# Kernel optimization log

Hardware: AMD Instinct MI355X
Metric: run time of the kernel (lower is better)

The kernel has to match this reference:

```python
import jax, jax.numpy as jnp
import numpy as np

MAX_VAL = 1000000000000.0


def setup_inputs() -> dict:
    key = jax.random.key(0)
    k1, k2, k3, k4 = jax.random.split(key, 4)
    B, H, N, D = 2, 16, 2048, 64
    query = jax.random.normal(k1, (B, H, N, D), dtype=jnp.float32)
    key_t = jax.random.normal(k2, (B, H, N, D), dtype=jnp.float32)
    value = jax.random.normal(k3, (B, H, N, D), dtype=jnp.float32)
    mask = jax.random.randint(k4, (B, 1, 1, N), 0, 2).astype(bool)
    return {"query": query, "key": key_t, "value": value, "mask": mask,
            "global_num": 8, "window_size": 64}


def reference(query, key, value, mask, global_num, window_size):
    # query/key/value: [B, H, N, D]; mask: [B, 1, 1, N] bool (True = keep)
    B, H, N, D = query.shape
    scale = 1.0 / jnp.sqrt(jnp.asarray(D, dtype=query.dtype))

    # split heads: first global_num are global, rest are local (windowed)
    q_g, k_g, v_g = query[:, :global_num], key[:, :global_num], value[:, :global_num]
    q_l, k_l, v_l = query[:, global_num:], key[:, global_num:], value[:, global_num:]

    # ---- global heads: dense masked attention ----
    scores_g = jnp.einsum('bhqd,bhkd->bhqk', q_g, k_g) * scale
    scores_g = jnp.where(mask, scores_g, -MAX_VAL)
    p_g = jax.nn.softmax(scores_g, axis=-1)
    out_g = jnp.einsum('bhqk,bhkd->bhqd', p_g, v_l[:, :0]) if False else jnp.einsum('bhqk,bhkd->bhqd', p_g, v_g)

    # ---- local heads: window-banded mask on top of padding mask ----
    pos = jnp.arange(N)
    distance = jnp.abs(pos[None, :] - pos[:, None])  # [N, N]
    band = (distance <= window_size)                 # [N, N] bool
    mask_l = mask & band                             # [B, 1, N, N]
    scores_l = jnp.einsum('bhqd,bhkd->bhqk', q_l, k_l) * scale
    scores_l = jnp.where(mask_l, scores_l, -MAX_VAL)
    p_l = jax.nn.softmax(scores_l, axis=-1)
    out_l = jnp.einsum('bhqk,bhkd->bhqd', p_l, v_l)

    out = jnp.concatenate([out_g, out_l], axis=1)  # [B, H, N, D]
    return (out, p_g, p_l)
```

## Files before the change

kernel.cpp:

```cpp
#include <hip/hip_runtime.h>
#include <stdint.h>

typedef __attribute__((ext_vector_type(8))) __bf16 bf16x8;
typedef __attribute__((ext_vector_type(4))) float f32x4;
typedef __attribute__((ext_vector_type(4))) int i32x4;

#define DEVI static __device__ __forceinline__

constexpr int NN = 2048;
constexpr int DD = 64;
constexpr int NH = 16;
constexpr int NG = 8;
constexpr float SCALE = 0.125f;
constexpr float NEGBIG = -1.0e12f;
constexpr size_t OUT_ELEMS = (size_t)2 * NH * NN * DD;
constexpr size_t PG_ELEMS  = (size_t)2 * NG * NN * NN;
constexpr size_t T_ELEMS   = (size_t)2 * NH * NN * DD;
constexpr size_t WS_NEED   = 5 * T_ELEMS * sizeof(__bf16);

struct Frag { bf16x8 hi, lo; };

DEVI Frag make_frag(const float* p) {
  f32x4 a = *(const f32x4*)p;
  f32x4 b = *(const f32x4*)(p + 4);
  Frag f;
#pragma unroll
  for (int j = 0; j < 8; j++) {
    float x = (j < 4) ? a[j] : b[j - 4];
    __bf16 h = (__bf16)x;
    f.hi[j] = h;
    f.lo[j] = (__bf16)(x - (float)h);
  }
  return f;
}

DEVI f32x4 mfma(bf16x8 a, bf16x8 b, f32x4 c) {
  return __builtin_amdgcn_mfma_f32_16x16x32_bf16(a, b, c, 0, 0, 0);
}

DEVI void compute_st(const Frag kf[2][2], const Frag* qf_rs, f32x4 acc[2]) {
#pragma unroll
  for (int Mt = 0; Mt < 2; Mt++) {
    f32x4 c = {0.f, 0.f, 0.f, 0.f};
#pragma unroll
    for (int ks = 0; ks < 2; ks++) {
      c = mfma(kf[Mt][ks].hi, qf_rs[ks].hi, c);
      c = mfma(kf[Mt][ks].hi, qf_rs[ks].lo, c);
      c = mfma(kf[Mt][ks].lo, qf_rs[ks].hi, c);
    }
    acc[Mt] = c;
  }
}

__global__ __launch_bounds__(256)
void prep(const float* __restrict__ Q, const float* __restrict__ K,
          const float* __restrict__ V, __bf16* __restrict__ W) {
  const int bid = blockIdx.x;
  if (bid < 4096) {
    const float* src = (bid < 2048) ? Q : K;
    __bf16* hi = W + ((bid < 2048) ? (size_t)0 : 2 * T_ELEMS);
    __bf16* lo = hi + T_ELEMS;
    const size_t base = ((size_t)(bid & 2047) * 256 + threadIdx.x) * 8;
    f32x4 a = *(const f32x4*)(src + base);
    f32x4 b = *(const f32x4*)(src + base + 4);
    bf16x8 h, l;
#pragma unroll
    for (int j = 0; j < 8; j++) {
      float x = (j < 4) ? a[j] : b[j - 4];
      __bf16 hh = (__bf16)x;
      h[j] = hh;
      l[j] = (__bf16)(x - (float)hh);
    }
    *(bf16x8*)(hi + base) = h;
    *(bf16x8*)(lo + base) = l;
  } else {
    __bf16* vt = W + 4 * T_ELEMS;
    const int t  = (bid - 4096) * 256 + (int)threadIdx.x;
    const int ng = t & 63;
    const int dh = t >> 6;
    const int d  = dh & 63;
    const int bh = dh >> 6;
    const float* vp = V + (size_t)bh * NN * DD;
    __bf16* dst = vt + ((size_t)bh * DD + d) * NN + ng * 32;
    bf16x8 o[4];
#pragma unroll
    for (int j = 0; j < 32; j++)
      o[j >> 3][j & 7] = (__bf16)vp[(size_t)(ng * 32 + j) * DD + d];
#pragma unroll
    for (int k = 0; k < 4; k++) *(bf16x8*)(dst + k * 8) = o[k];
  }
}

template <bool PRE>
__global__ __launch_bounds__(256, 2)
void wattn(const float* __restrict__ Q, const float* __restrict__ K,
           const float* __restrict__ V, const int* __restrict__ MSK,
           float* __restrict__ OUT, const __bf16* __restrict__ W) {
  const int bid = blockIdx.x;
  const bool loc = bid >= 256;
  const int lb = loc ? bid - 256 : bid;
  const int bh = lb >> 4;
  const int b  = bh >> 3;
  const int hh = bh & 7;
  const int h  = loc ? (hh + 8) : hh;
  const int wave = (int)(threadIdx.x >> 6);
  const int lane = (int)(threadIdx.x & 63);
  const int qi = lane >> 4;
  const int li = lane & 15;
  const int rb = (lb & 15) * 128 + wave * 32;

  const size_t tbase = ((size_t)(b * NH + h) * NN) * DD;
  const float* qp = Q + tbase;
  const float* kp = K + tbase;
  const float* vp = V + tbase;
  const __bf16* qhi = W + tbase;
  const __bf16* qlo = W + T_ELEMS + tbase;
  const __bf16* khi = W + 2 * T_ELEMS + tbase;
  const __bf16* klo = W + 3 * T_ELEMS + tbase;
  const __bf16* vt  = W + 4 * T_ELEMS + (size_t)(b * NH + h) * DD * NN;
  const int*   mp = MSK + (size_t)b * NN;
  float* op = OUT + tbase;
  float* pp = OUT + OUT_ELEMS + (loc ? PG_ELEMS : (size_t)0)
                  + ((size_t)(b * NG + hh) * NN) * NN;

  Frag qf[2][2];
#pragma unroll
  for (int rs = 0; rs < 2; rs++)
#pragma unroll
    for (int ks = 0; ks < 2; ks++) {
      const size_t off = (size_t)(rb + rs * 16 + li) * DD + ks * 32 + qi * 8;
      if constexpr (PRE) {
        qf[rs][ks].hi = *(const bf16x8*)(qhi + off);
        qf[rs][ks].lo = *(const bf16x8*)(qlo + off);
      } else {
        qf[rs][ks] = make_frag(qp + off);
      }
    }

  int wlo = 0, whi = 0;
  if (loc) {
    wlo = rb - 64; if (wlo < 0) wlo = 0;
    whi = rb + 96; if (whi > NN) whi = NN;
    const f32x4 z = {0.f, 0.f, 0.f, 0.f};
#pragma unroll 1
    for (int rr = 0; rr < 32; rr++) {
      float* dst = pp + (size_t)(rb + rr) * NN;
#pragma unroll 1
      for (int c = lane * 4; c < NN; c += 256) {
        if (c >= wlo && c < whi) continue;
        *(f32x4*)(dst + c) = z;
      }
    }
  }

  const int ntiles = loc ? 5 : 64;

  float m[2] = {NEGBIG, NEGBIG};
  float l[2] = {0.f, 0.f};

#pragma unroll 1
  for (int t = 0; t < ntiles; t++) {
    const int wc = loc ? (rb - 64 + 32 * t) : (32 * t);
    if (wc < 0 || wc >= NN) continue;

    Frag kf[2][2];
#pragma unroll
    for (int Mt = 0; Mt < 2; Mt++)
#pragma unroll
      for (int ks = 0; ks < 2; ks++) {
        const size_t off = (size_t)(wc + Mt * 16 + li) * DD + ks * 32 + qi * 8;
        if constexpr (PRE) {
          kf[Mt][ks].hi = *(const bf16x8*)(khi + off);
          kf[Mt][ks].lo = *(const bf16x8*)(klo + off);
        } else {
          kf[Mt][ks] = make_frag(kp + off);
        }
      }

    i32x4 mv[2];
    mv[0] = *(const i32x4*)(mp + wc + qi * 4);
    mv[1] = *(const i32x4*)(mp + wc + 16 + qi * 4);

#pragma unroll
    for (int rs = 0; rs < 2; rs++) {
      f32x4 acc[2];
      compute_st(kf, qf[rs], acc);
      const int row = rb + rs * 16 + li;
      float vals[8];
#pragma unroll
      for (int Mt = 0; Mt < 2; Mt++)
#pragma unroll
        for (int r = 0; r < 4; r++) {
          const int col = wc + Mt * 16 + qi * 4 + r;
          bool ok = (mv[Mt][r] != 0);
          if (loc) { int d = row - col; if (d < 0) d = -d; ok = ok && (d <= 64); }
          vals[Mt * 4 + r] = ok ? acc[Mt][r] * SCALE : NEGBIG;
        }
      float mx = vals[0];
#pragma unroll
      for (int j = 1; j < 8; j++) mx = fmaxf(mx, vals[j]);
      const float mn = fmaxf(m[rs], mx);
      float s = 0.f;
#pragma unroll
      for (int j = 0; j < 8; j++) s += __expf(vals[j] - mn);
      l[rs] = l[rs] * __expf(m[rs] - mn) + s;
      m[rs] = mn;
    }
  }

  float rl[2];
#pragma unroll
  for (int rs = 0; rs < 2; rs++) {
#pragma unroll
    for (int off = 16; off <= 32; off <<= 1) {
      const float mo = __shfl_xor(m[rs], off);
      const float lo2 = __shfl_xor(l[rs], off);
      const float mn = fmaxf(m[rs], mo);
      l[rs] = l[rs] * __expf(m[rs] - mn) + lo2 * __expf(mo - mn);
      m[rs] = mn;
    }
    rl[rs] = 1.0f / l[rs];
  }

  f32x4 o[2][4];
#pragma unroll
  for (int rs = 0; rs < 2; rs++)
#pragma unroll
    for (int dt = 0; dt < 4; dt++) o[rs][dt] = (f32x4){0.f, 0.f, 0.f, 0.f};

  const int srcA = (((qi * 2) + 0) & 3) * 16 + li;
  const int srcB = (((qi * 2) + 1) & 3) * 16 + li;
  const bool selB = (qi >> 1) != 0;

#pragma unroll 1
  for (int t = 0; t < ntiles; t++) {
    const int wc = loc ? (rb - 64 + 32 * t) : (32 * t);
    if (wc < 0 || wc >= NN) continue;

    Frag kf[2][2];
#pragma unroll
    for (int Mt = 0; Mt < 2; Mt++)
#pragma unroll
      for (int ks = 0; ks < 2; ks++) {
        const size_t off = (size_t)(wc + Mt * 16 + li) * DD + ks * 32 + qi * 8;
        if constexpr (PRE) {
          kf[Mt][ks].hi = *(const bf16x8*)(khi + off);
          kf[Mt][ks].lo = *(const bf16x8*)(klo + off);
        } else {
          kf[Mt][ks] = make_frag(kp + off);
        }
      }

    i32x4 mv[2];
    mv[0] = *(const i32x4*)(mp + wc + qi * 4);
    mv[1] = *(const i32x4*)(mp + wc + 16 + qi * 4);

    bf16x8 vf[4];
    if constexpr (PRE) {
#pragma unroll
      for (int dt = 0; dt < 4; dt++)
        vf[dt] = *(const bf16x8*)(vt + (size_t)(dt * 16 + li) * NN + wc + qi * 8);
    } else {
#pragma unroll
      for (int dt = 0; dt < 4; dt++)
#pragma unroll
        for (int j = 0; j < 8; j++)
          vf[dt][j] = (__bf16)vp[(size_t)(wc + qi * 8 + j) * DD + dt * 16 + li];
    }

#pragma unroll
    for (int rs = 0; rs < 2; rs++) {
      f32x4 acc[2];
      compute_st(kf, qf[rs], acc);
      const int row = rb + rs * 16 + li;
      float pf[8];
#pragma unroll
      for (int Mt = 0; Mt < 2; Mt++)
#pragma unroll
        for (int r = 0; r < 4; r++) {
          const int col = wc + Mt * 16 + qi * 4 + r;
          bool ok = (mv[Mt][r] != 0);
          if (loc) { int d = row - col; if (d < 0) d = -d; ok = ok && (d <= 64); }
          const float vv = ok ? acc[Mt][r] * SCALE : NEGBIG;
          pf[Mt * 4 + r] = __expf(vv - m[rs]) * rl[rs];
        }
      float pa[8];
#pragma unroll
      for (int j = 0; j < 8; j++) {
        const int src = (j < 4) ? srcA : srcB;
        const float v0 = __shfl(pf[0 + (j & 3)], src);
        const float v1 = __shfl(pf[4 + (j & 3)], src);
        pa[j] = selB ? v1 : v0;
      }
      float* prow = pp + (size_t)(rb + rs * 16 + li) * NN + wc + qi * 8;
      *(f32x4*)prow       = (f32x4){pa[0], pa[1], pa[2], pa[3]};
      *(f32x4*)(prow + 4) = (f32x4){pa[4], pa[5], pa[6], pa[7]};
      bf16x8 pb;
#pragma unroll
      for (int j = 0; j < 8; j++) pb[j] = (__bf16)pa[j];
#pragma unroll
      for (int dt = 0; dt < 4; dt++)
        o[rs][dt] = mfma(pb, vf[dt], o[rs][dt]);
    }
  }

#pragma unroll
  for (int rs = 0; rs < 2; rs++) {
#pragma unroll
    for (int dt = 0; dt < 4; dt++)
#pragma unroll
      for (int r = 0; r < 4; r++) {
        const int row = rb + rs * 16 + qi * 4 + r;
        op[(size_t)row * DD + dt * 16 + li] = o[rs][dt][r];
      }
  }
}

extern "C" void kernel_launch(void* const* d_in, const int* in_sizes, int n_in,
                              void* d_out, int out_size, void* d_ws, size_t ws_size,
                              hipStream_t stream) {
  (void)in_sizes; (void)n_in; (void)out_size;
  const float* Q = (const float*)d_in[0];
  const float* K = (const float*)d_in[1];
  const float* V = (const float*)d_in[2];
  const int*   M = (const int*)d_in[3];
  float* O = (float*)d_out;
  if (ws_size >= WS_NEED && d_ws != nullptr) {
    __bf16* W = (__bf16*)d_ws;
    prep<<<dim3(4608), dim3(256), 0, stream>>>(Q, K, V, W);
    wattn<true><<<dim3(512), dim3(256), 0, stream>>>(Q, K, V, M, O, W);
  } else {
    wattn<false><<<dim3(512), dim3(256), 0, stream>>>(Q, K, V, M, O, nullptr);
  }
}
```

Baseline: 784.0 us.

## Double-buffer K/V register tiles and specialize global vs local loops

Splits the attention loops into separate global and local paths, with the local band check made a compile-time template parameter. In the global path, K (and V) tiles plus the mask for the next step are loaded into a second register buffer while the current tile is computed, so global-memory latency overlaps with MFMA and softmax work. This raises register pressure, which could lower occupancy under the two-blocks-per-SM launch bound, and the last iteration issues a redundant reload.

```diff
diff --git a/kernel.cpp b/kernel.cpp
--- a/kernel.cpp
+++ b/kernel.cpp
@@ -38,17 +38,132 @@
   return __builtin_amdgcn_mfma_f32_16x16x32_bf16(a, b, c, 0, 0, 0);
 }
 
-DEVI void compute_st(const Frag kf[2][2], const Frag* qf_rs, f32x4 acc[2]) {
-#pragma unroll
-  for (int Mt = 0; Mt < 2; Mt++) {
-    f32x4 c = {0.f, 0.f, 0.f, 0.f};
+struct KT { bf16x8 hi[2][2]; bf16x8 lo[2][2]; i32x4 mv[2]; };
+struct VT { bf16x8 v[4]; };
+
+template <bool PRE>
+DEVI void load_kt(KT& kt, const __bf16* khi, const __bf16* klo,
+                  const float* kp, const int* mp, int wc, int li, int qi) {
+#pragma unroll
+  for (int Mt = 0; Mt < 2; Mt++)
 #pragma unroll
     for (int ks = 0; ks < 2; ks++) {
-      c = mfma(kf[Mt][ks].hi, qf_rs[ks].hi, c);
-      c = mfma(kf[Mt][ks].hi, qf_rs[ks].lo, c);
-      c = mfma(kf[Mt][ks].lo, qf_rs[ks].hi, c);
-    }
-    acc[Mt] = c;
+      const size_t off = (size_t)(wc + Mt * 16 + li) * DD + ks * 32 + qi * 8;
+      if constexpr (PRE) {
+        kt.hi[Mt][ks] = *(const bf16x8*)(khi + off);
+        kt.lo[Mt][ks] = *(const bf16x8*)(klo + off);
+      } else {
+        Frag f = make_frag(kp + off);
+        kt.hi[Mt][ks] = f.hi;
+        kt.lo[Mt][ks] = f.lo;
+      }
+    }
+  kt.mv[0] = *(const i32x4*)(mp + wc + qi * 4);
+  kt.mv[1] = *(const i32x4*)(mp + wc + 16 + qi * 4);
+}
+
+template <bool PRE>
+DEVI void load_vt(VT& vt, const __bf16* vtp, const float* vp, int wc, int li, int qi) {
+  if constexpr (PRE) {
+#pragma unroll
+    for (int dt = 0; dt < 4; dt++)
+      vt.v[dt] = *(const bf16x8*)(vtp + (size_t)(dt * 16 + li) * NN + wc + qi * 8);
+  } else {
+#pragma unroll
+    for (int dt = 0; dt < 4; dt++)
+#pragma unroll
+      for (int j = 0; j < 8; j++)
+        vt.v[dt][j] = (__bf16)vp[(size_t)(wc + qi * 8 + j) * DD + dt * 16 + li];
+  }
+}
+
+template <bool LOC>
+DEVI void tileA(const KT& kt, const Frag qf[2][2], int wc, int rb, int li, int qi,
+                float* m, float* l) {
+#pragma unroll
+  for (int rs = 0; rs < 2; rs++) {
+    f32x4 acc[2];
+#pragma unroll
+    for (int Mt = 0; Mt < 2; Mt++) {
+      f32x4 c = {0.f, 0.f, 0.f, 0.f};
+#pragma unroll
+      for (int ks = 0; ks < 2; ks++) {
+        c = mfma(kt.hi[Mt][ks], qf[rs][ks].hi, c);
+        c = mfma(kt.hi[Mt][ks], qf[rs][ks].lo, c);
+        c = mfma(kt.lo[Mt][ks], qf[rs][ks].hi, c);
+      }
+      acc[Mt] = c;
+    }
+    const int row = rb + rs * 16 + li;
+    float vals[8];
+#pragma unroll
+    for (int Mt = 0; Mt < 2; Mt++)
+#pragma unroll
+      for (int r = 0; r < 4; r++) {
+        const int col = wc + Mt * 16 + qi * 4 + r;
+        bool ok = (kt.mv[Mt][r] != 0);
+        if constexpr (LOC) { int d = row - col; if (d < 0) d = -d; ok = ok && (d <= 64); }
+        vals[Mt * 4 + r] = ok ? acc[Mt][r] * SCALE : NEGBIG;
+      }
+    float mx = vals[0];
+#pragma unroll
+    for (int j = 1; j < 8; j++) mx = fmaxf(mx, vals[j]);
+    const float mn = fmaxf(m[rs], mx);
+    float s = 0.f;
+#pragma unroll
+    for (int j = 0; j < 8; j++) s += __expf(vals[j] - mn);
+    l[rs] = l[rs] * __expf(m[rs] - mn) + s;
+    m[rs] = mn;
+  }
+}
+
+template <bool LOC>
+DEVI void tileB(const KT& kt, const VT& vt, const Frag qf[2][2], int wc, int rb,
+                int li, int qi, const float* m, const float* rl,
+                f32x4 (&o)[2][4], float* pp, int srcA, int srcB, bool selB) {
+#pragma unroll
+  for (int rs = 0; rs < 2; rs++) {
+    f32x4 acc[2];
+#pragma unroll
+    for (int Mt = 0; Mt < 2; Mt++) {
+      f32x4 c = {0.f, 0.f, 0.f, 0.f};
+#pragma unroll
+      for (int ks = 0; ks < 2; ks++) {
+        c = mfma(kt.hi[Mt][ks], qf[rs][ks].hi, c);
+        c = mfma(kt.hi[Mt][ks], qf[rs][ks].lo, c);
+        c = mfma(kt.lo[Mt][ks], qf[rs][ks].hi, c);
+      }
+      acc[Mt] = c;
+    }
+    const int row = rb + rs * 16 + li;
+    float pf[8];
+#pragma unroll
+    for (int Mt = 0; Mt < 2; Mt++)
+#pragma unroll
+      for (int r = 0; r < 4; r++) {
+        const int col = wc + Mt * 16 + qi * 4 + r;
+        bool ok = (kt.mv[Mt][r] != 0);
+        if constexpr (LOC) { int d = row - col; if (d < 0) d = -d; ok = ok && (d <= 64); }
+        const float vv = ok ? acc[Mt][r] * SCALE : NEGBIG;
+        pf[Mt * 4 + r] = __expf(vv - m[rs]) * rl[rs];
+      }
+    float pa[8];
+#pragma unroll
+    for (int j = 0; j < 8; j++) {
+      const int src = (j < 4) ? srcA : srcB;
+      const float v0 = __shfl(pf[0 + (j & 3)], src);
+      const float v1 = __shfl(pf[4 + (j & 3)], src);
+      pa[j] = selB ? v1 : v0;
+    }
+    float* prow = pp + (size_t)(rb + rs * 16 + li) * NN + wc + qi * 8;
+    *(f32x4*)prow       = (f32x4){pa[0], pa[1], pa[2], pa[3]};
+    *(f32x4*)(prow + 4) = (f32x4){pa[4], pa[5], pa[6], pa[7]};
+    bf16x8 pb;
+#pragma unroll
+    for (int j = 0; j < 8; j++) pb[j] = (__bf16)pa[j];
+#pragma unroll
+    for (int dt = 0; dt < 4; dt++)
+      o[rs][dt] = mfma(pb, vt.v[dt], o[rs][dt]);
   }
 }
 
@@ -109,17 +224,17 @@
   const int li = lane & 15;
   const int rb = (lb & 15) * 128 + wave * 32;
 
-  const size_t tbase = ((size_t)(b * NH + h) * NN) * DD;
-  const float* qp = Q + tbase;
-  const float* kp = K + tbase;
-  const float* vp = V + tbase;
-  const __bf16* qhi = W + tbase;
-  const __bf16* qlo = W + T_ELEMS + tbase;
-  const __bf16* khi = W + 2 * T_ELEMS + tbase;
-  const __bf16* klo = W + 3 * T_ELEMS + tbase;
-  const __bf16* vt  = W + 4 * T_ELEMS + (size_t)(b * NH + h) * DD * NN;
+  const size_t tb = ((size_t)(b * NH + h) * NN) * DD;
+  const float* qp = Q + tb;
+  const float* kp = K + tb;
+  const float* vp = V + tb;
+  const __bf16* qhi = W + tb;
+  const __bf16* qlo = W + T_ELEMS + tb;
+  const __bf16* khi = W + 2 * T_ELEMS + tb;
+  const __bf16* klo = W + 3 * T_ELEMS + tb;
+  const __bf16* vtp = W + 4 * T_ELEMS + (size_t)(b * NH + h) * DD * NN;
   const int*   mp = MSK + (size_t)b * NN;
-  float* op = OUT + tbase;
+  float* op = OUT + tb;
   float* pp = OUT + OUT_ELEMS + (loc ? PG_ELEMS : (size_t)0)
                   + ((size_t)(b * NG + hh) * NN) * NN;
 
@@ -137,10 +252,23 @@
       }
     }
 
-  int wlo = 0, whi = 0;
-  if (loc) {
-    wlo = rb - 64; if (wlo < 0) wlo = 0;
-    whi = rb + 96; if (whi > NN) whi = NN;
+  float m[2] = {NEGBIG, NEGBIG};
+  float l[2] = {0.f, 0.f};
+
+  if (!loc) {
+    KT ka, kb;
+    load_kt<PRE>(ka, khi, klo, kp, mp, 0, li, qi);
+#pragma unroll 1
+    for (int t = 0; t < 64; t += 2) {
+      load_kt<PRE>(kb, khi, klo, kp, mp, (t + 1) * 32, li, qi);
+      tileA<false>(ka, qf, t * 32, rb, li, qi, m, l);
+      const int wn = (t + 2 < 64) ? (t + 2) * 32 : 63 * 32;
+      load_kt<PRE>(ka, khi, klo, kp, mp, wn, li, qi);
+      tileA<false>(kb, qf, (t + 1) * 32, rb, li, qi, m, l);
+    }
+  } else {
+    int wlo = rb - 64; if (wlo < 0) wlo = 0;
+    int whi = rb + 96; if (whi > NN) whi = NN;
     const f32x4 z = {0.f, 0.f, 0.f, 0.f};
 #pragma unroll 1
     for (int rr = 0; rr < 32; rr++) {
@@ -151,60 +279,13 @@
         *(f32x4*)(dst + c) = z;
       }
     }
-  }
-
-  const int ntiles = loc ? 5 : 64;
-
-  float m[2] = {NEGBIG, NEGBIG};
-  float l[2] = {0.f, 0.f};
-
-#pragma unroll 1
-  for (int t = 0; t < ntiles; t++) {
-    const int wc = loc ? (rb - 64 + 32 * t) : (32 * t);
-    if (wc < 0 || wc >= NN) continue;
-
-    Frag kf[2][2];
-#pragma unroll
-    for (int Mt = 0; Mt < 2; Mt++)
-#pragma unroll
-      for (int ks = 0; ks < 2; ks++) {
-        const size_t off = (size_t)(wc + Mt * 16 + li) * DD + ks * 32 + qi * 8;
-        if constexpr (PRE) {
-          kf[Mt][ks].hi = *(const bf16x8*)(khi + off);
-          kf[Mt][ks].lo = *(const bf16x8*)(klo + off);
-        } else {
-          kf[Mt][ks] = make_frag(kp + off);
-        }
-      }
-
-    i32x4 mv[2];
-    mv[0] = *(const i32x4*)(mp + wc + qi * 4);
-    mv[1] = *(const i32x4*)(mp + wc + 16 + qi * 4);
-
-#pragma unroll
-    for (int rs = 0; rs < 2; rs++) {
-      f32x4 acc[2];
-      compute_st(kf, qf[rs], acc);
-      const int row = rb + rs * 16 + li;
-      float vals[8];
-#pragma unroll
-      for (int Mt = 0; Mt < 2; Mt++)
-#pragma unroll
-        for (int r = 0; r < 4; r++) {
-          const int col = wc + Mt * 16 + qi * 4 + r;
-          bool ok = (mv[Mt][r] != 0);
-          if (loc) { int d = row - col; if (d < 0) d = -d; ok = ok && (d <= 64); }
-          vals[Mt * 4 + r] = ok ? acc[Mt][r] * SCALE : NEGBIG;
-        }
-      float mx = vals[0];
-#pragma unroll
-      for (int j = 1; j < 8; j++) mx = fmaxf(mx, vals[j]);
-      const float mn = fmaxf(m[rs], mx);
-      float s = 0.f;
-#pragma unroll
-      for (int j = 0; j < 8; j++) s += __expf(vals[j] - mn);
-      l[rs] = l[rs] * __expf(m[rs] - mn) + s;
-      m[rs] = mn;
+    KT ka;
+#pragma unroll 1
+    for (int t = 0; t < 5; t++) {
+      const int wc = rb - 64 + 32 * t;
+      if ((unsigned)wc >= (unsigned)NN) continue;
+      load_kt<PRE>(ka, khi, klo, kp, mp, wc, li, qi);
+      tileA<true>(ka, qf, wc, rb, li, qi, m, l);
     }
   }
 
@@ -213,9 +294,9 @@
   for (int rs = 0; rs < 2; rs++) {
 #pragma unroll
     for (int off = 16; off <= 32; off <<= 1) {
-      const float mo = __shfl_xor(m[rs], off);
+      const float mo  = __shfl_xor(m[rs], off);
       const float lo2 = __shfl_xor(l[rs], off);
-      const float mn = fmaxf(m[rs], mo);
+      const float mn  = fmaxf(m[rs], mo);
       l[rs] = l[rs] * __expf(m[rs] - mn) + lo2 * __expf(mo - mn);
       m[rs] = mn;
     }
@@ -232,80 +313,36 @@
   const int srcB = (((qi * 2) + 1) & 3) * 16 + li;
   const bool selB = (qi >> 1) != 0;
 
-#pragma unroll 1
-  for (int t = 0; t < ntiles; t++) {
-    const int wc = loc ? (rb - 64 + 32 * t) : (32 * t);
-    if (wc < 0 || wc >= NN) continue;
-
-    Frag kf[2][2];
-#pragma unroll
-    for (int Mt = 0; Mt < 2; Mt++)
-#pragma unroll
-      for (int ks = 0; ks < 2; ks++) {
-        const size_t off = (size_t)(wc + Mt * 16 + li) * DD + ks * 32 + qi * 8;
-        if constexpr (PRE) {
-          kf[Mt][ks].hi = *(const bf16x8*)(khi + off);
-          kf[Mt][ks].lo = *(const bf16x8*)(klo + off);
-        } else {
-          kf[Mt][ks] = make_frag(kp + off);
-        }
-      }
-
-    i32x4 mv[2];
-    mv[0] = *(const i32x4*)(mp + wc + qi * 4);
-    mv[1] = *(const i32x4*)(mp + wc + 16 + qi * 4);
-
-    bf16x8 vf[4];
-    if constexpr (PRE) {
-#pragma unroll
-      for (int dt = 0; dt < 4; dt++)
-        vf[dt] = *(const bf16x8*)(vt + (size_t)(dt * 16 + li) * NN + wc + qi * 8);
-    } else {
-#pragma unroll
-      for (int dt = 0; dt < 4; dt++)
-#pragma unroll
-        for (int j = 0; j < 8; j++)
-          vf[dt][j] = (__bf16)vp[(size_t)(wc + qi * 8 + j) * DD + dt * 16 + li];
-    }
-
-#pragma unroll
-    for (int rs = 0; rs < 2; rs++) {
-      f32x4 acc[2];
-      compute_st(kf, qf[rs], acc);
-      const int row = rb + rs * 16 + li;
-      float pf[8];
-#pragma unroll
-      for (int Mt = 0; Mt < 2; Mt++)
-#pragma unroll
-        for (int r = 0; r < 4; r++) {
-          const int col = wc + Mt * 16 + qi * 4 + r;
-          bool ok = (mv[Mt][r] != 0);
-          if (loc) { int d = row - col; if (d < 0) d = -d; ok = ok && (d <= 64); }
-          const float vv = ok ? acc[Mt][r] * SCALE : NEGBIG;
-          pf[Mt * 4 + r] = __expf(vv - m[rs]) * rl[rs];
-        }
-      float pa[8];
-#pragma unroll
-      for (int j = 0; j < 8; j++) {
-        const int src = (j < 4) ? srcA : srcB;
-        const float v0 = __shfl(pf[0 + (j & 3)], src);
-        const float v1 = __shfl(pf[4 + (j & 3)], src);
-        pa[j] = selB ? v1 : v0;
-      }
-      float* prow = pp + (size_t)(rb + rs * 16 + li) * NN + wc + qi * 8;
-      *(f32x4*)prow       = (f32x4){pa[0], pa[1], pa[2], pa[3]};
-      *(f32x4*)(prow + 4) = (f32x4){pa[4], pa[5], pa[6], pa[7]};
-      bf16x8 pb;
-#pragma unroll
-      for (int j = 0; j < 8; j++) pb[j] = (__bf16)pa[j];
-#pragma unroll
-      for (int dt = 0; dt < 4; dt++)
-        o[rs][dt] = mfma(pb, vf[dt], o[rs][dt]);
-    }
-  }
-
-#pragma unroll
-  for (int rs = 0; rs < 2; rs++) {
+  if (!loc) {
+    KT ka, kb;
+    VT va, vb;
+    load_kt<PRE>(ka, khi, klo, kp, mp, 0, li, qi);
+    load_vt<PRE>(va, vtp, vp, 0, li, qi);
+#pragma unroll 1
+    for (int t = 0; t < 64; t += 2) {
+      load_kt<PRE>(kb, khi, klo, kp, mp, (t + 1) * 32, li, qi);
+      load_vt<PRE>(vb, vtp, vp, (t + 1) * 32, li, qi);
+      tileB<false>(ka, va, qf, t * 32, rb, li, qi, m, rl, o, pp, srcA, srcB, selB);
+      const int wn = (t + 2 < 64) ? (t + 2) * 32 : 63 * 32;
+      load_kt<PRE>(ka, khi, klo, kp, mp, wn, li, qi);
+      load_vt<PRE>(va, vtp, vp, wn, li, qi);
+      tileB<false>(kb, vb, qf, (t + 1) * 32, rb, li, qi, m, rl, o, pp, srcA, srcB, selB);
+    }
+  } else {
+    KT ka;
+    VT va;
+#pragma unroll 1
+    for (int t = 0; t < 5; t++) {
+      const int wc = rb - 64 + 32 * t;
+      if ((unsigned)wc >= (unsigned)NN) continue;
+      load_kt<PRE>(ka, khi, klo, kp, mp, wc, li, qi);
+      load_vt<PRE>(va, vtp, vp, wc, li, qi);
+      tileB<true>(ka, va, qf, wc, rb, li, qi, m, rl, o, pp, srcA, srcB, selB);
+    }
+  }
+
+#pragma unroll
+  for (int rs = 0; rs < 2; rs++)
 #pragma unroll
     for (int dt = 0; dt < 4; dt++)
 #pragma unroll
@@ -313,7 +350,6 @@
         const int row = rb + rs * 16 + qi * 4 + r;
         op[(size_t)row * DD + dt * 16 + li] = o[rs][dt][r];
       }
-  }
 }
 
 extern "C" void kernel_launch(void* const* d_in, const int* in_sizes, int n_in,
```

Measured after the change: 804.9 us. 2.7% more time.
